# Optimization experiments

Hardware: AMD Instinct MI355X
Metric: run time of the kernel (lower is better)

Reference implementation:

```python
import jax, jax.numpy as jnp
import numpy as np

ROPE_BASE = 10000.0

def rope_2d(x, h, w):
    # x: (b, h, w, c); 2D RoPE, first half of pair-channels rotated by row angle, second by col angle
    b, _, _, c = x.shape
    k_max = c // 4  # c // (2 * num_spatial_dims)
    theta = 1.0 / (ROPE_BASE ** (jnp.arange(k_max, dtype=jnp.float32) / k_max))  # (k_max,)
    ang_h = jnp.arange(h, dtype=jnp.float32)[:, None] * theta  # (h, k_max)
    ang_w = jnp.arange(w, dtype=jnp.float32)[:, None] * theta  # (w, k_max)
    # angles: (h, w, 2*k_max) = cat([i*theta, j*theta], -1)
    angles = jnp.concatenate([
        jnp.broadcast_to(ang_h[:, None, :], (h, w, k_max)),
        jnp.broadcast_to(ang_w[None, :, :], (h, w, k_max)),
    ], axis=-1)
    cos = jnp.cos(angles)  # (h, w, c//2)
    sin = jnp.sin(angles)
    xr = x[..., 0::2]  # consecutive-pair real parts (b,h,w,c//2)
    xi = x[..., 1::2]
    out_r = xr * cos - xi * sin
    out_i = xr * sin + xi * cos
    return jnp.stack([out_r, out_i], axis=-1).reshape(b, h, w, c)

def linear_attention_fwd(x, h, w, qk_w, qk_b, lepe_w, lepe_b, num_heads=4):
    b, n, c = x.shape
    head_dim = c // num_heads
    qk = x @ qk_w.T + qk_b  # (b, n, 2c)
    q, k = qk[..., :c], qk[..., c:]
    v = x
    q = jax.nn.elu(q) + 1.0
    k = jax.nn.elu(k) + 1.0
    q_rope = rope_2d(q.reshape(b, h, w, c), h, w).reshape(b, n, num_heads, head_dim).transpose(0, 2, 1, 3)
    k_rope = rope_2d(k.reshape(b, h, w, c), h, w).reshape(b, n, num_heads, head_dim).transpose(0, 2, 1, 3)
    qh = q.reshape(b, n, num_heads, head_dim).transpose(0, 2, 1, 3)  # (b,H,n,d)
    kh = k.reshape(b, n, num_heads, head_dim).transpose(0, 2, 1, 3)
    vh = v.reshape(b, n, num_heads, head_dim).transpose(0, 2, 1, 3)
    k_mean = kh.mean(axis=2)  # (b,H,d)
    z = 1.0 / (jnp.einsum('bhnd,bhd->bhn', qh, k_mean) + 1e-6)  # (b,H,n)
    inv_n = 1.0 / n
    kv = jnp.einsum('bhnd,bhne->bhde', k_rope, vh) * inv_n  # (b,H,d,d)
    out = jnp.einsum('bhnd,bhde->bhne', q_rope, kv) * z[..., None]  # (b,H,n,d)
    out = out.transpose(0, 2, 1, 3).reshape(b, n, c)
    # LePE: depthwise 3x3 conv on v in NCHW
    v_img = v.reshape(b, h, w, c).transpose(0, 3, 1, 2)  # (b,c,h,w)
    lepe = jax.lax.conv_general_dilated(
        v_img, lepe_w, window_strides=(1, 1), padding='SAME',
        feature_group_count=c, dimension_numbers=('NCHW', 'OIHW', 'NCHW'))
    lepe = lepe + lepe_b[None, :, None, None]
    out = out + lepe.transpose(0, 2, 3, 1).reshape(b, n, c)
    return out.transpose(0, 2, 1).reshape(b, c, h, w)

def setup_inputs() -> dict:
    key = jax.random.key(0)
    ks = jax.random.split(key, 5)
    b, h, w, c = 16, 128, 128, 64
    n = h * w
    x = jax.random.normal(ks[0], (b, n, c), dtype=jnp.float32)
    qk_w = jax.random.normal(ks[1], (2 * c, c), dtype=jnp.float32) * (1.0 / np.sqrt(c))
    qk_b = jax.random.normal(ks[2], (2 * c,), dtype=jnp.float32) * 0.02
    lepe_w = jax.random.normal(ks[3], (c, 1, 3, 3), dtype=jnp.float32) * (1.0 / 3.0)
    lepe_b = jax.random.normal(ks[4], (c,), dtype=jnp.float32) * 0.02
    return {"x": x, "h": h, "w": w, "qk_w": qk_w, "qk_b": qk_b, "lepe_w": lepe_w, "lepe_b": lepe_b}

def reference(x, h, w, qk_w, qk_b, lepe_w, lepe_b):
    return linear_attention_fwd(x, h, w, qk_w, qk_b, lepe_w, lepe_b, num_heads=4)
```

## Files before the change

kernel.cpp:

```cpp
#include <hip/hip_runtime.h>

#define B_   16
#define C_   64
#define HH   128
#define WW   128
#define NN   (HH*WW)
#define NH   4
#define HD   16
#define PADB 72
#define PADO 66

typedef short short8 __attribute__((ext_vector_type(8)));
typedef short short4v __attribute__((ext_vector_type(4)));
typedef float f32x4  __attribute__((ext_vector_type(4)));

__device__ __forceinline__ float act_elu1(float v) {
    return v > 0.f ? v + 1.f : __expf(v);
}
__device__ __forceinline__ short f2bf(float f) {
    union { float f; unsigned u; } v; v.f = f;
    unsigned r = (v.u + 0x7FFFu + ((v.u >> 16) & 1u)) >> 16;
    return (short)r;
}

#define NEG_L2_10K_OVER16 (-0.8304820237218406f)

__global__ __launch_bounds__(256) void la_phase1(
    const float* __restrict__ x, const float* __restrict__ qk_w,
    const float* __restrict__ qk_b, float* __restrict__ g_part)
{
    __shared__ __align__(16) char pool[4*64*PADB*2 + 256*4];
    short* sW  = (short*)pool;
    short* sX  = sW  + 64*PADB;
    short* sXT = sX  + 64*PADB;
    short* sKT = sXT + 64*PADB;
    float* kmp = (float*)(sKT + 64*PADB);

    const int tid  = threadIdx.x;
    const int w    = tid >> 6;
    const int ln   = tid & 15;
    const int quad = (tid >> 4) & 3;
    const int b    = blockIdx.y;
    const int nblk = blockIdx.x;
    const float* xb = x + (size_t)b * (size_t)(NN * C_);

    #pragma unroll
    for (int it = 0; it < 4; ++it) {
        int idx = tid + 256*it;
        int row = idx & 63, k4 = (idx >> 6) << 2;
        float4 wv = *(const float4*)(qk_w + (64 + row)*64 + k4);
        short4v s4 = { f2bf(wv.x), f2bf(wv.y), f2bf(wv.z), f2bf(wv.w) };
        *(short4v*)(sW + row*PADB + k4) = s4;
    }

    float bias[4];
    #pragma unroll
    for (int nt = 0; nt < 4; ++nt) bias[nt] = qk_b[64 + 16*nt + ln];

    f32x4 acc2 = {0.f, 0.f, 0.f, 0.f};
    float kmacc[4] = {0.f, 0.f, 0.f, 0.f};

    for (int ck = 0; ck < 4; ++ck) {
        const int n0 = nblk*256 + ck*64;
        if (ck) __syncthreads();
        #pragma unroll
        for (int it = 0; it < 4; ++it) {
            int idx = tid + 256*it;
            int row = idx & 63, k4 = (idx >> 6) << 2;
            float4 xv = *(const float4*)(xb + (size_t)(n0 + row)*C_ + k4);
            short4v s4 = { f2bf(xv.x), f2bf(xv.y), f2bf(xv.z), f2bf(xv.w) };
            *(short4v*)(sX + row*PADB + k4) = s4;
            sXT[(k4+0)*PADB + row] = s4.x;
            sXT[(k4+1)*PADB + row] = s4.y;
            sXT[(k4+2)*PADB + row] = s4.z;
            sXT[(k4+3)*PADB + row] = s4.w;
        }
        __syncthreads();

        f32x4 acc[4];
        #pragma unroll
        for (int nt = 0; nt < 4; ++nt) acc[nt] = (f32x4){0.f,0.f,0.f,0.f};
        #pragma unroll
        for (int ks = 0; ks < 2; ++ks) {
            short8 a = *(const short8*)(sX + (16*w + ln)*PADB + 32*ks + 8*quad);
            #pragma unroll
            for (int nt = 0; nt < 4; ++nt) {
                short8 bf = *(const short8*)(sW + (16*nt + ln)*PADB + 32*ks + 8*quad);
                acc[nt] = __builtin_amdgcn_mfma_f32_16x16x32_bf16(a, bf, acc[nt], 0, 0, 0);
            }
        }

        #pragma unroll
        for (int nt = 0; nt < 4; ++nt) {
            const int j = 16*nt + ln;
            const int t = j >> 1;
            const float theta = exp2f(NEG_L2_10K_OVER16 * (float)(t & 15));
            const bool isY = (t < 16);
            const float sgn = (j & 1) ? 1.f : -1.f;
            #pragma unroll
            for (int r = 0; r < 4; ++r) {
                float kval = act_elu1(acc[nt][r] + bias[nt]);
                kmacc[nt] += kval;
                float P = __shfl_xor(kval, 1);
                int p_loc = 16*w + 4*quad + r;
                int n = n0 + p_loc;
                float coord = isY ? (float)(n >> 7) : (float)(n & 127);
                float s, c;
                __sincosf(coord * theta, &s, &c);
                float kr = kval*c + sgn*P*s;
                sKT[j*PADB + p_loc] = f2bf(kr);
            }
        }
        __syncthreads();

        #pragma unroll
        for (int ks = 0; ks < 2; ++ks) {
            short8 a  = *(const short8*)(sKT + (16*w + ln)*PADB + 32*ks + 8*quad);
            short8 bf = *(const short8*)(sXT + (16*w + ln)*PADB + 32*ks + 8*quad);
            acc2 = __builtin_amdgcn_mfma_f32_16x16x32_bf16(a, bf, acc2, 0, 0, 0);
        }
    }

    float* pb = g_part + (size_t)(b*64 + nblk) * 1088;
    #pragma unroll
    for (int r = 0; r < 4; ++r)
        pb[w*256 + (4*quad + r)*16 + ln] = acc2[r];

    #pragma unroll
    for (int nt = 0; nt < 4; ++nt) {
        float v = kmacc[nt];
        v += __shfl_xor(v, 16);
        v += __shfl_xor(v, 32);
        if ((tid & 63) < 16) kmp[w*64 + 16*nt + ln] = v;
    }
    __syncthreads();
    if (tid < 64)
        pb[1024 + tid] = kmp[tid] + kmp[64 + tid] + kmp[128 + tid] + kmp[192 + tid];
}

__global__ __launch_bounds__(256) void la_reduce(
    const float* __restrict__ g_part, float* __restrict__ g_kv,
    float* __restrict__ g_km)
{
    int o = blockIdx.x * 256 + threadIdx.x;
    int b = o / 1088;
    int i = o - b * 1088;
    const float* p = g_part + (size_t)(b*64) * 1088 + i;
    float s = 0.f;
    #pragma unroll 8
    for (int nb = 0; nb < 64; ++nb) s += p[(size_t)nb * 1088];
    if (i < 1024) g_kv[b*1024 + i] = s;
    else          g_km[b*64 + (i - 1024)] = s;
}

__global__ __launch_bounds__(256) void la_phase2(
    const float* __restrict__ x, const float* __restrict__ qk_w,
    const float* __restrict__ qk_b, const float* __restrict__ lepe_w,
    const float* __restrict__ lepe_b, const float* __restrict__ g_kv,
    const float* __restrict__ g_km, float* __restrict__ out)
{
    __shared__ __align__(16) char pool[32768];
    short* sX   = (short*)pool;
    short* sW   = sX + 64*PADB;
    float* sOut = (float*)pool;
    short* sQ   = (short*)(pool + 18432);
    short* sKVB = sQ + 64*PADB;

    const int tid  = threadIdx.x;
    const int w    = tid >> 6;
    const int ln   = tid & 15;
    const int quad = (tid >> 4) & 3;
    const int b    = blockIdx.y;
    const int n0   = blockIdx.x * 64;
    const float* xb = x + (size_t)b * (size_t)(NN * C_);
    const float inv_n = 1.f / (float)NN;

    #pragma unroll
    for (int it = 0; it < 4; ++it) {
        int idx = tid + 256*it;
        int row = idx & 63, k4 = (idx >> 6) << 2;
        float4 xv = *(const float4*)(xb + (size_t)(n0 + row)*C_ + k4);
        short4v s4 = { f2bf(xv.x), f2bf(xv.y), f2bf(xv.z), f2bf(xv.w) };
        *(short4v*)(sX + row*PADB + k4) = s4;
        float4 wv = *(const float4*)(qk_w + row*64 + k4);
        short4v s5 = { f2bf(wv.x), f2bf(wv.y), f2bf(wv.z), f2bf(wv.w) };
        *(short4v*)(sW + row*PADB + k4) = s5;
    }
    for (int idx = tid; idx < 1024; idx += 256) {
        int h = idx >> 8, d = (idx >> 4) & 15, e = idx & 15;
        float v = g_kv[b*1024 + idx] * inv_n;
        int rowb = h*16 + e;
        int kpos  = (h & 1) ? 16 + d : d;
        int kzero = (h & 1) ? d : 16 + d;
        sKVB[rowb*40 + kpos]  = f2bf(v);
        sKVB[rowb*40 + kzero] = 0;
    }
    float biasq[4], kmv[4];
    #pragma unroll
    for (int nt = 0; nt < 4; ++nt) {
        biasq[nt] = qk_b[16*nt + ln];
        kmv[nt]   = g_km[b*64 + 16*nt + ln];
    }
    __syncthreads();

    f32x4 acc[4];
    #pragma unroll
    for (int nt = 0; nt < 4; ++nt) acc[nt] = (f32x4){0.f,0.f,0.f,0.f};
    #pragma unroll
    for (int ks = 0; ks < 2; ++ks) {
        short8 a = *(const short8*)(sX + (16*w + ln)*PADB + 32*ks + 8*quad);
        #pragma unroll
        for (int nt = 0; nt < 4; ++nt) {
            short8 bf = *(const short8*)(sW + (16*nt + ln)*PADB + 32*ks + 8*quad);
            acc[nt] = __builtin_amdgcn_mfma_f32_16x16x32_bf16(a, bf, acc[nt], 0, 0, 0);
        }
    }

    float z_all[4][4];
    #pragma unroll
    for (int nt = 0; nt < 4; ++nt) {
        const int j = 16*nt + ln;
        const int t = j >> 1;
        const float theta = exp2f(NEG_L2_10K_OVER16 * (float)(t & 15));
        const bool isY = (t < 16);
        const float sgn = (j & 1) ? 1.f : -1.f;
        #pragma unroll
        for (int r = 0; r < 4; ++r) {
            float qval = act_elu1(acc[nt][r] + biasq[nt]);
            float dotp = qval * kmv[nt];
            dotp += __shfl_xor(dotp, 1);
            dotp += __shfl_xor(dotp, 2);
            dotp += __shfl_xor(dotp, 4);
            dotp += __shfl_xor(dotp, 8);
            z_all[nt][r] = 1.f / (dotp * inv_n + 1e-6f);
            float P = __shfl_xor(qval, 1);
            int p_loc = 16*w + 4*quad + r;
            int n = n0 + p_loc;
            float coord = isY ? (float)(n >> 7) : (float)(n & 127);
            float s, c;
            __sincosf(coord * theta, &s, &c);
            float qr = qval*c + sgn*P*s;
            sQ[p_loc*PADB + j] = f2bf(qr);
        }
    }
    __syncthreads();

    f32x4 accq[4];
    #pragma unroll
    for (int h = 0; h < 4; ++h) accq[h] = (f32x4){0.f,0.f,0.f,0.f};
    #pragma unroll
    for (int P2 = 0; P2 < 2; ++P2) {
        short8 a = *(const short8*)(sQ + (16*w + ln)*PADB + 32*P2 + 8*quad);
        #pragma unroll
        for (int hh = 0; hh < 2; ++hh) {
            int h = 2*P2 + hh;
            short8 bf = *(const short8*)(sKVB + (h*16 + ln)*40 + 8*quad);
            accq[h] = __builtin_amdgcn_mfma_f32_16x16x32_bf16(a, bf, accq[h], 0, 0, 0);
        }
    }
    #pragma unroll
    for (int h = 0; h < 4; ++h)
        #pragma unroll
        for (int r = 0; r < 4; ++r)
            sOut[(16*h + ln)*PADO + 16*w + 4*quad + r] = accq[h][r] * z_all[h][r];
    __syncthreads();

    const int ch = tid >> 2, sub = tid & 3, p0 = 16*sub;
    const int yy = n0 >> 7, xbase = n0 & 127, gx0 = xbase + p0;
    float wv9[9];
    #pragma unroll
    for (int tap = 0; tap < 9; ++tap) wv9[tap] = lepe_w[ch*9 + tap];
    const float lb = lepe_b[ch];
    float accl[16];
    #pragma unroll
    for (int j = 0; j < 16; ++j) accl[j] = 0.f;
    #pragma unroll
    for (int dy = -1; dy <= 1; ++dy) {
        int y2 = yy + dy;
        if ((unsigned)y2 >= HH) continue;
        const float* rp = xb + (size_t)(y2*WW)*C_ + ch;
        float cb[18];
        #pragma unroll
        for (int jj = 0; jj < 18; ++jj) {
            int col = gx0 - 1 + jj;
            cb[jj] = ((unsigned)col < WW) ? rp[(size_t)col*C_] : 0.f;
        }
        float w0 = wv9[(dy+1)*3 + 0], w1 = wv9[(dy+1)*3 + 1], w2 = wv9[(dy+1)*3 + 2];
        #pragma unroll
        for (int j = 0; j < 16; ++j)
            accl[j] += cb[j]*w0 + cb[j+1]*w1 + cb[j+2]*w2;
    }
    float* outp = out + (size_t)b*(size_t)(C_*NN) + (size_t)ch*NN + n0 + p0;
    #pragma unroll
    for (int g = 0; g < 4; ++g) {
        float2 a0 = *(const float2*)(sOut + ch*PADO + p0 + 4*g);
        float2 a1 = *(const float2*)(sOut + ch*PADO + p0 + 4*g + 2);
        float4 o4 = { a0.x + accl[4*g+0] + lb, a0.y + accl[4*g+1] + lb,
                      a1.x + accl[4*g+2] + lb, a1.y + accl[4*g+3] + lb };
        *(float4*)(outp + 4*g) = o4;
    }
}

extern "C" void kernel_launch(void* const* d_in, const int* in_sizes, int n_in,
                              void* d_out, int out_size, void* d_ws, size_t ws_size,
                              hipStream_t stream) {
    const float* x      = (const float*)d_in[0];
    const float* qk_w   = (const float*)d_in[3];
    const float* qk_b   = (const float*)d_in[4];
    const float* lepe_w = (const float*)d_in[5];
    const float* lepe_b = (const float*)d_in[6];
    float* out = (float*)d_out;

    float* g_part = (float*)d_ws;
    float* g_kv   = g_part + 1024*1088;
    float* g_km   = g_kv + 16*1024;

    hipLaunchKernelGGL(la_phase1, dim3(64, B_), dim3(256), 0, stream,
                       x, qk_w, qk_b, g_part);
    hipLaunchKernelGGL(la_reduce, dim3(68), dim3(256), 0, stream,
                       g_part, g_kv, g_km);
    hipLaunchKernelGGL(la_phase2, dim3(256, B_), dim3(256), 0, stream,
                       x, qk_w, qk_b, lepe_w, lepe_b, g_kv, g_km, out);
}
```

Baseline: 197.8 us.

## Keep phase1 weights in registers, load MFMA A from global, precompute RoPE table

Phase1 now holds the bf16 K-projection weight fragments in registers instead of LDS. It builds the MFMA A operand directly from global x loads rather than staging a row-major copy in LDS. The transposed x tile is written with vectorized short4 stores. A new init kernel precomputes a cos/sin table in workspace, so phase1 reads a table entry instead of calling sincos per element. This trades LDS traffic, barriers and transcendental work for an extra kernel launch, duplicate global reads of x and more registers. An extra barrier is also added in phase2.

```diff
diff --git a/kernel.cpp b/kernel.cpp
--- a/kernel.cpp
+++ b/kernel.cpp
@@ -4,15 +4,14 @@
 #define C_   64
 #define HH   128
 #define WW   128
-#define NN   (HH*WW)
-#define NH   4
-#define HD   16
+#define NN   16384
+#define PADT 72
 #define PADB 72
 #define PADO 66
 
-typedef short short8 __attribute__((ext_vector_type(8)));
+typedef short short8  __attribute__((ext_vector_type(8)));
 typedef short short4v __attribute__((ext_vector_type(4)));
-typedef float f32x4  __attribute__((ext_vector_type(4)));
+typedef float f32x4   __attribute__((ext_vector_type(4)));
 
 __device__ __forceinline__ float act_elu1(float v) {
     return v > 0.f ? v + 1.f : __expf(v);
@@ -22,80 +21,102 @@
     unsigned r = (v.u + 0x7FFFu + ((v.u >> 16) & 1u)) >> 16;
     return (short)r;
 }
+__device__ __forceinline__ short8 pack8(float4 a, float4 b) {
+    short8 r;
+    r[0]=f2bf(a.x); r[1]=f2bf(a.y); r[2]=f2bf(a.z); r[3]=f2bf(a.w);
+    r[4]=f2bf(b.x); r[5]=f2bf(b.y); r[6]=f2bf(b.z); r[7]=f2bf(b.w);
+    return r;
+}
 
 #define NEG_L2_10K_OVER16 (-0.8304820237218406f)
+
+#define WS_KV   1114112
+#define WS_KM   1130496
+#define WS_TBL  1131520
+
+__global__ void init_kernel(float* __restrict__ ws) {
+    int e = blockIdx.x * 256 + threadIdx.x;
+    if (e < 2048) {
+        int coord = e >> 4, t = e & 15;
+        float theta = exp2f(NEG_L2_10K_OVER16 * (float)t);
+        float s, c;
+        sincosf((float)coord * theta, &s, &c);
+        ws[WS_TBL + 2*e]     = c;
+        ws[WS_TBL + 2*e + 1] = s;
+    }
+}
 
 __global__ __launch_bounds__(256) void la_phase1(
     const float* __restrict__ x, const float* __restrict__ qk_w,
-    const float* __restrict__ qk_b, float* __restrict__ g_part)
+    const float* __restrict__ qk_b, float* __restrict__ ws)
 {
-    __shared__ __align__(16) char pool[4*64*PADB*2 + 256*4];
-    short* sW  = (short*)pool;
-    short* sX  = sW  + 64*PADB;
-    short* sXT = sX  + 64*PADB;
-    short* sKT = sXT + 64*PADB;
-    float* kmp = (float*)(sKT + 64*PADB);
+    __shared__ __align__(16) short sXT[64*PADT];
+    __shared__ __align__(16) short sKT[64*PADT];
+    __shared__ float kmp[256];
 
     const int tid  = threadIdx.x;
     const int w    = tid >> 6;
     const int ln   = tid & 15;
     const int quad = (tid >> 4) & 3;
     const int b    = blockIdx.y;
-    const int nblk = blockIdx.x;
-    const float* xb = x + (size_t)b * (size_t)(NN * C_);
-
-    #pragma unroll
-    for (int it = 0; it < 4; ++it) {
-        int idx = tid + 256*it;
-        int row = idx & 63, k4 = (idx >> 6) << 2;
-        float4 wv = *(const float4*)(qk_w + (64 + row)*64 + k4);
-        short4v s4 = { f2bf(wv.x), f2bf(wv.y), f2bf(wv.z), f2bf(wv.w) };
-        *(short4v*)(sW + row*PADB + k4) = s4;
-    }
-
+    const float* xb = x + (size_t)b * (size_t)(NN * 64);
+    const float2* tbl = (const float2*)(ws + WS_TBL);
+    float* g_part = ws;
+
+    short8 wf[2][4];
+    #pragma unroll
+    for (int ks = 0; ks < 2; ++ks)
+        #pragma unroll
+        for (int nt = 0; nt < 4; ++nt) {
+            const float* p = qk_w + (size_t)(64 + 16*nt + ln)*64 + 32*ks + 8*quad;
+            wf[ks][nt] = pack8(*(const float4*)p, *(const float4*)(p+4));
+        }
     float bias[4];
     #pragma unroll
     for (int nt = 0; nt < 4; ++nt) bias[nt] = qk_b[64 + 16*nt + ln];
 
-    f32x4 acc2 = {0.f, 0.f, 0.f, 0.f};
-    float kmacc[4] = {0.f, 0.f, 0.f, 0.f};
+    f32x4 acc2 = {0.f,0.f,0.f,0.f};
+    float kmacc[4] = {0.f,0.f,0.f,0.f};
+
+    const int sp = 4*(tid & 15);
+    const int sc = 4*(tid >> 4);
 
     for (int ck = 0; ck < 4; ++ck) {
-        const int n0 = nblk*256 + ck*64;
+        const int n0 = blockIdx.x*256 + ck*64;
         if (ck) __syncthreads();
-        #pragma unroll
-        for (int it = 0; it < 4; ++it) {
-            int idx = tid + 256*it;
-            int row = idx & 63, k4 = (idx >> 6) << 2;
-            float4 xv = *(const float4*)(xb + (size_t)(n0 + row)*C_ + k4);
-            short4v s4 = { f2bf(xv.x), f2bf(xv.y), f2bf(xv.z), f2bf(xv.w) };
-            *(short4v*)(sX + row*PADB + k4) = s4;
-            sXT[(k4+0)*PADB + row] = s4.x;
-            sXT[(k4+1)*PADB + row] = s4.y;
-            sXT[(k4+2)*PADB + row] = s4.z;
-            sXT[(k4+3)*PADB + row] = s4.w;
-        }
-        __syncthreads();
+
+        {
+            float4 r0 = *(const float4*)(xb + (size_t)(n0+sp+0)*64 + sc);
+            float4 r1 = *(const float4*)(xb + (size_t)(n0+sp+1)*64 + sc);
+            float4 r2 = *(const float4*)(xb + (size_t)(n0+sp+2)*64 + sc);
+            float4 r3 = *(const float4*)(xb + (size_t)(n0+sp+3)*64 + sc);
+            short4v t0 = { f2bf(r0.x), f2bf(r1.x), f2bf(r2.x), f2bf(r3.x) };
+            short4v t1 = { f2bf(r0.y), f2bf(r1.y), f2bf(r2.y), f2bf(r3.y) };
+            short4v t2 = { f2bf(r0.z), f2bf(r1.z), f2bf(r2.z), f2bf(r3.z) };
+            short4v t3 = { f2bf(r0.w), f2bf(r1.w), f2bf(r2.w), f2bf(r3.w) };
+            *(short4v*)(sXT + (sc+0)*PADT + sp) = t0;
+            *(short4v*)(sXT + (sc+1)*PADT + sp) = t1;
+            *(short4v*)(sXT + (sc+2)*PADT + sp) = t2;
+            *(short4v*)(sXT + (sc+3)*PADT + sp) = t3;
+        }
 
         f32x4 acc[4];
         #pragma unroll
         for (int nt = 0; nt < 4; ++nt) acc[nt] = (f32x4){0.f,0.f,0.f,0.f};
         #pragma unroll
         for (int ks = 0; ks < 2; ++ks) {
-            short8 a = *(const short8*)(sX + (16*w + ln)*PADB + 32*ks + 8*quad);
+            const float* ap = xb + (size_t)(n0 + 16*w + ln)*64 + 32*ks + 8*quad;
+            short8 a = pack8(*(const float4*)ap, *(const float4*)(ap+4));
             #pragma unroll
-            for (int nt = 0; nt < 4; ++nt) {
-                short8 bf = *(const short8*)(sW + (16*nt + ln)*PADB + 32*ks + 8*quad);
-                acc[nt] = __builtin_amdgcn_mfma_f32_16x16x32_bf16(a, bf, acc[nt], 0, 0, 0);
-            }
+            for (int nt = 0; nt < 4; ++nt)
+                acc[nt] = __builtin_amdgcn_mfma_f32_16x16x32_bf16(a, wf[ks][nt], acc[nt], 0, 0, 0);
         }
 
         #pragma unroll
         for (int nt = 0; nt < 4; ++nt) {
-            const int j = 16*nt + ln;
-            const int t = j >> 1;
-            const float theta = exp2f(NEG_L2_10K_OVER16 * (float)(t & 15));
-            const bool isY = (t < 16);
+            const int j  = 16*nt + ln;
+            const int tq = (j >> 1) & 15;
+            const bool isY = (j >> 1) < 16;
             const float sgn = (j & 1) ? 1.f : -1.f;
             #pragma unroll
             for (int r = 0; r < 4; ++r) {
@@ -104,24 +125,23 @@
                 float P = __shfl_xor(kval, 1);
                 int p_loc = 16*w + 4*quad + r;
                 int n = n0 + p_loc;
-                float coord = isY ? (float)(n >> 7) : (float)(n & 127);
-                float s, c;
-                __sincosf(coord * theta, &s, &c);
-                float kr = kval*c + sgn*P*s;
-                sKT[j*PADB + p_loc] = f2bf(kr);
+                int coord = isY ? (n >> 7) : (n & 127);
+                float2 cs = tbl[coord*16 + tq];
+                float kr = kval*cs.x + sgn*P*cs.y;
+                sKT[j*PADT + p_loc] = f2bf(kr);
             }
         }
         __syncthreads();
 
         #pragma unroll
         for (int ks = 0; ks < 2; ++ks) {
-            short8 a  = *(const short8*)(sKT + (16*w + ln)*PADB + 32*ks + 8*quad);
-            short8 bf = *(const short8*)(sXT + (16*w + ln)*PADB + 32*ks + 8*quad);
-            acc2 = __builtin_amdgcn_mfma_f32_16x16x32_bf16(a, bf, acc2, 0, 0, 0);
-        }
-    }
-
-    float* pb = g_part + (size_t)(b*64 + nblk) * 1088;
+            short8 a  = *(const short8*)(sKT + (16*w + ln)*PADT + 32*ks + 8*quad);
+            short8 bb = *(const short8*)(sXT + (16*w + ln)*PADT + 32*ks + 8*quad);
+            acc2 = __builtin_amdgcn_mfma_f32_16x16x32_bf16(a, bb, acc2, 0, 0, 0);
+        }
+    }
+
+    float* pb = g_part + (size_t)(b*64 + blockIdx.x) * 1088;
     #pragma unroll
     for (int r = 0; r < 4; ++r)
         pb[w*256 + (4*quad + r)*16 + ln] = acc2[r];
@@ -189,7 +209,7 @@
     for (int idx = tid; idx < 1024; idx += 256) {
         int h = idx >> 8, d = (idx >> 4) & 15, e = idx & 15;
         float v = g_kv[b*1024 + idx] * inv_n;
-        int rowb = h*16 + e;
+        int rowb  = h*16 + e;
         int kpos  = (h & 1) ? 16 + d : d;
         int kzero = (h & 1) ? d : 16 + d;
         sKVB[rowb*40 + kpos]  = f2bf(v);
@@ -219,7 +239,7 @@
     float z_all[4][4];
     #pragma unroll
     for (int nt = 0; nt < 4; ++nt) {
-        const int j = 16*nt + ln;
+        const int j  = 16*nt + ln;
         const int t = j >> 1;
         const float theta = exp2f(NEG_L2_10K_OVER16 * (float)(t & 15));
         const bool isY = (t < 16);
@@ -258,6 +278,8 @@
             accq[h] = __builtin_amdgcn_mfma_f32_16x16x32_bf16(a, bf, accq[h], 0, 0, 0);
         }
     }
+    __syncthreads();
+
     #pragma unroll
     for (int h = 0; h < 4; ++h)
         #pragma unroll
@@ -290,7 +312,7 @@
         for (int j = 0; j < 16; ++j)
             accl[j] += cb[j]*w0 + cb[j+1]*w1 + cb[j+2]*w2;
     }
-    float* outp = out + (size_t)b*(size_t)(C_*NN) + (size_t)ch*NN + n0 + p0;
+    float* outp = out + ((size_t)(b*64 + ch))*NN + n0 + p0;
     #pragma unroll
     for (int g = 0; g < 4; ++g) {
         float2 a0 = *(const float2*)(sOut + ch*PADO + p0 + 4*g);
@@ -310,15 +332,15 @@
     const float* lepe_w = (const float*)d_in[5];
     const float* lepe_b = (const float*)d_in[6];
     float* out = (float*)d_out;
-
-    float* g_part = (float*)d_ws;
-    float* g_kv   = g_part + 1024*1088;
-    float* g_km   = g_kv + 16*1024;
-
-    hipLaunchKernelGGL(la_phase1, dim3(64, B_), dim3(256), 0, stream,
-                       x, qk_w, qk_b, g_part);
-    hipLaunchKernelGGL(la_reduce, dim3(68), dim3(256), 0, stream,
-                       g_part, g_kv, g_km);
+    float* ws  = (float*)d_ws;
+
+    float* g_part = ws;
+    float* g_kv   = ws + WS_KV;
+    float* g_km   = ws + WS_KM;
+
+    hipLaunchKernelGGL(init_kernel, dim3(8), dim3(256), 0, stream, ws);
+    hipLaunchKernelGGL(la_phase1, dim3(64, B_), dim3(256), 0, stream, x, qk_w, qk_b, ws);
+    hipLaunchKernelGGL(la_reduce, dim3(68), dim3(256), 0, stream, g_part, g_kv, g_km);
     hipLaunchKernelGGL(la_phase2, dim3(256, B_), dim3(256), 0, stream,
                        x, qk_w, qk_b, lepe_w, lepe_b, g_kv, g_km, out);
 }
```

Result: slower. 216.8 us (+9.6%).
